# Optimization experiments

Hardware: AMD Instinct MI355X
Metric: run time of the kernel (lower is better)

## Reference

```python
import jax, jax.numpy as jnp
import numpy as np

HIDDEN = 2048
HEADS = 32
GROUPS = 8
HEAD_DIM = HIDDEN // HEADS  # 64
BSZ = 1
SEQ = 2048
KV_DIM = GROUPS * HEAD_DIM  # 512


def setup_inputs() -> dict:
    key = jax.random.key(0)
    ks = jax.random.split(key, 10)
    scale = 1.0 / np.sqrt(HIDDEN)
    x = jax.random.normal(ks[0], (BSZ, SEQ, HIDDEN), dtype=jnp.float32)
    # causal mask: 1 where attention is disallowed (strictly upper triangular)
    causal_mask = jnp.triu(jnp.ones((SEQ, SEQ), dtype=jnp.float32), k=1)
    Wq = jax.random.normal(ks[1], (HIDDEN, HIDDEN), dtype=jnp.float32) * scale
    bq = jnp.zeros((HIDDEN,), dtype=jnp.float32)
    Wk = jax.random.normal(ks[2], (HIDDEN, KV_DIM), dtype=jnp.float32) * scale
    bk = jnp.zeros((KV_DIM,), dtype=jnp.float32)
    Wv = jax.random.normal(ks[3], (HIDDEN, KV_DIM), dtype=jnp.float32) * scale
    bv = jnp.zeros((KV_DIM,), dtype=jnp.float32)
    Wo = jax.random.normal(ks[4], (HIDDEN, HIDDEN), dtype=jnp.float32) * scale
    bo = jnp.zeros((HIDDEN,), dtype=jnp.float32)
    return {"x": x, "causal_mask": causal_mask, "Wq": Wq, "bq": bq,
            "Wk": Wk, "bk": bk, "Wv": Wv, "bv": bv, "Wo": Wo, "bo": bo}


def reference(x, causal_mask, Wq, bq, Wk, bk, Wv, bv, Wo, bo):
    b, s, _ = x.shape
    r = HEADS // GROUPS  # queries per KV group
    # projections
    q = (x @ Wq + bq).reshape(b, s, HEADS, HEAD_DIM).transpose(0, 2, 1, 3)   # [b,H,s,d]
    k = (x @ Wk + bk).reshape(b, s, GROUPS, HEAD_DIM).transpose(0, 2, 1, 3)  # [b,G,s,d]
    v = (x @ Wv + bv).reshape(b, s, GROUPS, HEAD_DIM).transpose(0, 2, 1, 3)  # [b,G,s,d]
    # group query heads: head h belongs to group h // r (matches torch expand/reshape order)
    qg = q.reshape(b, GROUPS, r, s, HEAD_DIM)
    inv_sqrt_d = 1.0 / jnp.sqrt(jnp.float32(HEAD_DIM))
    # scores without physically expanding K/V across heads
    scores = jnp.einsum('bgrsd,bgtd->bgrst', qg, k) * inv_sqrt_d  # [b,G,r,s,t]
    scores = scores + causal_mask * (-1e9)
    attn = jax.nn.softmax(scores, axis=-1)
    out = jnp.einsum('bgrst,bgtd->bgrsd', attn, v)                 # [b,G,r,s,d]
    out = out.reshape(b, HEADS, s, HEAD_DIM).transpose(0, 2, 1, 3).reshape(b, s, HIDDEN)
    return out @ Wo + bo
```

## Files before the change

kernel.cpp:

```cpp
#include <hip/hip_runtime.h>

typedef __attribute__((ext_vector_type(8))) short short8;
typedef __attribute__((ext_vector_type(4))) float f32x4;
typedef unsigned short us4 __attribute__((ext_vector_type(4)));
typedef unsigned int u32x2 __attribute__((ext_vector_type(2)));

#define S_LEN 2048
#define HID   2048
#define KVD   512
#define NH    32
#define NG    8
#define HD    64

__device__ __forceinline__ float b2f(ushort u) {
  union { uint i; float f; } c; c.i = ((uint)u) << 16; return c.f;
}
__device__ __forceinline__ ushort f2b(float f) {
  union { float f; uint u; } c; c.f = f;
  uint u = c.u;
  uint r = (u + 0x7FFFu + ((u >> 16) & 1u)) >> 16;
  return (ushort)r;
}

__device__ __forceinline__ void gld_lds16(const ushort* g, short* l) {
  __builtin_amdgcn_global_load_lds(
      (const __attribute__((address_space(1))) void*)g,
      (__attribute__((address_space(3))) void*)l, 16, 0, 0);
}

__global__ __launch_bounds__(256) void detect_dtype(
    const uint* __restrict__ mask, int* __restrict__ flagp)
{
  __shared__ int s_f32;
  if (threadIdx.x == 0) s_f32 = 1;
  __syncthreads();
  int bad = 0;
  for (int i = threadIdx.x; i < 8192; i += 256) {
    const uint w = mask[i];
    if (w != 0u && w != 0x3F800000u) bad = 1;
  }
  if (bad) s_f32 = 0;
  __syncthreads();
  if (threadIdx.x == 0) *flagp = s_f32;
}

__global__ __launch_bounds__(256) void convert_x(
    const void* __restrict__ src, ushort* __restrict__ dst, int n,
    const int* __restrict__ flagp)
{
  const int i = (blockIdx.x * 256 + threadIdx.x) * 4;
  if (i >= n) return;
  if (*flagp) {
    const f32x4 v = *(const f32x4*)((const float*)src + i);
    us4 o;
    o.x = f2b(v.x); o.y = f2b(v.y); o.z = f2b(v.z); o.w = f2b(v.w);
    *(us4*)(dst + i) = o;
  } else {
    *(us4*)(dst + i) = *(const us4*)((const ushort*)src + i);
  }
}

__global__ __launch_bounds__(256) void transpose_any(
    const void* __restrict__ src, ushort* __restrict__ dst, int R, int C,
    const int* __restrict__ flagp)
{
  const int f32 = *flagp;
  __shared__ ushort tile[32][33];
  const int x  = blockIdx.x * 32 + threadIdx.x;
  const int y0 = blockIdx.y * 32;
  for (int i = threadIdx.y; i < 32; i += 8) {
    const size_t idx = (size_t)(y0 + i) * C + x;
    tile[i][threadIdx.x] = f32 ? f2b(((const float*)src)[idx])
                               : ((const ushort*)src)[idx];
  }
  __syncthreads();
  const int xo  = blockIdx.y * 32 + threadIdx.x;
  const int yo0 = blockIdx.x * 32;
  for (int i = threadIdx.y; i < 32; i += 8)
    dst[(size_t)(yo0 + i) * R + xo] = tile[threadIdx.x][i];
}

struct GemmRegions {
  const ushort* Bt[3];
  const void*   bias[3];
  void*         out[3];
  int   ldo[3];
  int   trans[3];
  int   outf32[3];
  float scale[3];
  int   colStart[3];
  int   colEnd[3];
};

__global__ __launch_bounds__(256) void gemm_bt_kernel(
    const ushort* __restrict__ A, int M, int K, GemmRegions rg,
    const int* __restrict__ flagp)
{
  __shared__ __align__(16) short As[2][128 * 32];
  __shared__ __align__(16) short Bs[2][128 * 32];

  const int tid  = threadIdx.x;
  const int wave = tid >> 6;
  const int lane = tid & 63;
  const int wm = wave & 1, wn = wave >> 1;
  const int quad = lane >> 4, l16 = lane & 15;

  const int rowBase = blockIdx.y * 128;
  const int colBase = blockIdx.x * 128;

  int ri = 0;
#pragma unroll
  for (int i = 0; i < 3; ++i)
    if (colBase >= rg.colStart[i] && colBase < rg.colEnd[i]) ri = i;

  const int colLocal0   = colBase - rg.colStart[ri];
  const ushort* BtBase  = rg.Bt[ri] + (size_t)colLocal0 * K;
  const void* bias      = rg.bias[ri];
  void* outp            = rg.out[ri];
  const int   ldo   = rg.ldo[ri];
  const int   trans = rg.trans[ri];
  const int   of32  = rg.outf32[ri];
  const float scale = rg.scale[ri];

  const int sRow = tid >> 2;
  const int sCol = (tid & 3) * 8;

  const ushort* a0 = A + (size_t)(rowBase + sRow) * K + sCol;
  const ushort* a1 = A + (size_t)(rowBase + sRow + 64) * K + sCol;
  const ushort* b0 = BtBase + (size_t)sRow * K + sCol;
  const ushort* b1 = BtBase + (size_t)(sRow + 64) * K + sCol;

  const int waveRow = wave * 16;

  f32x4 acc[4][4] = {};
  const int nt = K >> 5;

  gld_lds16(a0, &As[0][waveRow * 32]);
  gld_lds16(a1, &As[0][(waveRow + 64) * 32]);
  gld_lds16(b0, &Bs[0][waveRow * 32]);
  gld_lds16(b1, &Bs[0][(waveRow + 64) * 32]);
  __syncthreads();

  for (int t = 0; t < nt; ++t) {
    const int cur = t & 1;

    if (t + 1 < nt) {
      const int nb = cur ^ 1;
      const int k0 = (t + 1) * 32;
      gld_lds16(a0 + k0, &As[nb][waveRow * 32]);
      gld_lds16(a1 + k0, &As[nb][(waveRow + 64) * 32]);
      gld_lds16(b0 + k0, &Bs[nb][waveRow * 32]);
      gld_lds16(b1 + k0, &Bs[nb][(waveRow + 64) * 32]);
    }

    short8 af[4], bf[4];
#pragma unroll
    for (int mi = 0; mi < 4; ++mi)
      af[mi] = *(const short8*)&As[cur][(wm * 64 + mi * 16 + l16) * 32 + quad * 8];
#pragma unroll
    for (int ni = 0; ni < 4; ++ni)
      bf[ni] = *(const short8*)&Bs[cur][(wn * 64 + ni * 16 + l16) * 32 + quad * 8];

#pragma unroll
    for (int mi = 0; mi < 4; ++mi)
#pragma unroll
      for (int ni = 0; ni < 4; ++ni)
        acc[mi][ni] = __builtin_amdgcn_mfma_f32_16x16x32_bf16(
            af[mi], bf[ni], acc[mi][ni], 0, 0, 0);

    __syncthreads();
  }

  const int f32io = *flagp;

#pragma unroll
  for (int ni = 0; ni < 4; ++ni) {
    const int cl = wn * 64 + ni * 16 + l16;
    const float bv = f32io ? ((const float*)bias)[colLocal0 + cl]
                           : b2f(((const ushort*)bias)[colLocal0 + cl]);
#pragma unroll
    for (int mi = 0; mi < 4; ++mi) {
      const int row0 = rowBase + wm * 64 + mi * 16 + quad * 4;
#pragma unroll
      for (int r = 0; r < 4; ++r) {
        const float val = (acc[mi][ni][r] + bv) * scale;
        if (!trans) {
          const size_t off = (size_t)(row0 + r) * ldo + colLocal0 + cl;
          if (of32 && f32io) ((float*)outp)[off] = val;
          else               ((ushort*)outp)[off] = f2b(val);
        } else {
          ((ushort*)outp)[(size_t)(colLocal0 + cl) * M + row0 + r] = f2b(val);
        }
      }
    }
  }
}

#define PSTR 40

#define MFMA16(A, B, C) __builtin_amdgcn_mfma_f32_16x16x32_bf16(A, B, C, 0, 0, 0)

#define LOADKV(IT, K00, K01, K10, K11, V0, V1, V2, V3)                        \
  {                                                                           \
    int t0_ = (IT) * 32;                                                      \
    if (t0_ > S_LEN - 32) t0_ = S_LEN - 32;                                   \
    const ushort* kr0_ = Kb + (size_t)(t0_ + l16) * KVD + g * HD + quad * 8;  \
    const ushort* kr1_ = kr0_ + (size_t)16 * KVD;                             \
    K00 = *(const short8*)(kr0_);                                             \
    K01 = *(const short8*)(kr0_ + 32);                                        \
    K10 = *(const short8*)(kr1_);                                             \
    K11 = *(const short8*)(kr1_ + 32);                                        \
    const ushort* vr_ = Vt + (size_t)(g * 64 + l16) * S_LEN + t0_ + quad * 8; \
    V0 = *(const short8*)(vr_);                                               \
    V1 = *(const short8*)(vr_ + (size_t)16 * S_LEN);                          \
    V2 = *(const short8*)(vr_ + (size_t)32 * S_LEN);                          \
    V3 = *(const short8*)(vr_ + (size_t)48 * S_LEN);                          \
  }

#define COMPUTE(IT, K00, K01, K10, K11, V0, V1, V2, V3)                       \
  {                                                                           \
    const int t0_ = (IT) * 32;                                                \
    const bool edge_ = (IT) >= nfull;                                         \
    _Pragma("unroll")                                                         \
    for (int qf = 0; qf < 4; ++qf) {                                          \
      f32x4 z0 = {};                                                          \
      z0 = MFMA16(K00, qfB[qf][0], z0);                                       \
      z0 = MFMA16(K01, qfB[qf][1], z0);                                       \
      f32x4 z1 = {};                                                          \
      z1 = MFMA16(K10, qfB[qf][0], z1);                                       \
      z1 = MFMA16(K11, qfB[qf][1], z1);                                       \
      ushort p0[4], p1[4];                                                    \
      _Pragma("unroll")                                                       \
      for (int r = 0; r < 4; ++r) {                                           \
        float pv0 = __expf(z0[r]);                                            \
        float pv1 = __expf(z1[r]);                                            \
        if (edge_) {                                                          \
          const int qq_ = qbase + qf * 16 + l16;                              \
          if (t0_ + quad * 4 + r > qq_)      pv0 = 0.f;                       \
          if (t0_ + 16 + quad * 4 + r > qq_) pv1 = 0.f;                       \
        }                                                                     \
        p0[r] = f2b(pv0);                                                     \
        p1[r] = f2b(pv1);                                                     \
      }                                                                       \
      u32x2 w0, w1;                                                           \
      w0.x = (uint)p0[0] | ((uint)p0[1] << 16);                               \
      w0.y = (uint)p0[2] | ((uint)p0[3] << 16);                               \
      w1.x = (uint)p1[0] | ((uint)p1[1] << 16);                               \
      w1.y = (uint)p1[2] | ((uint)p1[3] << 16);                               \
      *(u32x2*)&pb[(qf * 16 + l16) * PSTR + quad * 4] = w0;                   \
      *(u32x2*)&pb[(qf * 16 + l16) * PSTR + 16 + quad * 4] = w1;              \
    }                                                                         \
    asm volatile("s_waitcnt lgkmcnt(0)" ::: "memory");                        \
    _Pragma("unroll")                                                         \
    for (int qf = 0; qf < 4; ++qf) {                                          \
      const short8 pa =                                                       \
          *(const short8*)&pb[(qf * 16 + l16) * PSTR + quad * 8];             \
      l_acc[qf] = MFMA16(pa, ones, l_acc[qf]);                                \
      o_acc[qf][0] = MFMA16(pa, V0, o_acc[qf][0]);                            \
      o_acc[qf][1] = MFMA16(pa, V1, o_acc[qf][1]);                            \
      o_acc[qf][2] = MFMA16(pa, V2, o_acc[qf][2]);                            \
      o_acc[qf][3] = MFMA16(pa, V3, o_acc[qf][3]);                            \
    }                                                                         \
  }

__global__ __launch_bounds__(256, 2) void attn_kernel(
    const ushort* __restrict__ Q, const ushort* __restrict__ Kb,
    const ushort* __restrict__ Vt, ushort* __restrict__ O)
{
  __shared__ __align__(16) short Pls[4][64 * PSTR];

  const int tid  = threadIdx.x;
  const int wave = tid >> 6;
  const int lane = tid & 63;
  const int quad = lane >> 4, l16 = lane & 15;

  const int h = blockIdx.y;
  const int g = h >> 2;
  const int qbase = blockIdx.x * 256 + wave * 64;

  short8 qfB[4][2];
#pragma unroll
  for (int qf = 0; qf < 4; ++qf) {
    const ushort* qr = Q + (size_t)(qbase + qf * 16 + l16) * HID + h * HD;
#pragma unroll
    for (int ks = 0; ks < 2; ++ks)
      qfB[qf][ks] = *(const short8*)(qr + ks * 32 + quad * 8);
  }

  short8 ones;
#pragma unroll
  for (int j = 0; j < 8; ++j) ones[j] = (short)0x3F80;

  f32x4 o_acc[4][4] = {};
  f32x4 l_acc[4] = {};

  short* pb = &Pls[wave][0];
  const int nfull = qbase >> 5;
  const int total = nfull + 2;

  short8 ka00, ka01, ka10, ka11, va0, va1, va2, va3;
  short8 kb00, kb01, kb10, kb11, vb0, vb1, vb2, vb3;

  LOADKV(0, ka00, ka01, ka10, ka11, va0, va1, va2, va3);
  for (int it = 0; it < total; it += 2) {
    LOADKV(it + 1, kb00, kb01, kb10, kb11, vb0, vb1, vb2, vb3);
    COMPUTE(it, ka00, ka01, ka10, ka11, va0, va1, va2, va3);
    LOADKV(it + 2, ka00, ka01, ka10, ka11, va0, va1, va2, va3);
    COMPUTE(it + 1, kb00, kb01, kb10, kb11, vb0, vb1, vb2, vb3);
  }

#pragma unroll
  for (int qf = 0; qf < 4; ++qf) {
    f32x4 linv;
#pragma unroll
    for (int r = 0; r < 4; ++r) linv[r] = 1.f / l_acc[qf][r];
#pragma unroll
    for (int df = 0; df < 4; ++df)
#pragma unroll
      for (int r = 0; r < 4; ++r)
        O[(size_t)(qbase + qf * 16 + quad * 4 + r) * HID + h * HD + df * 16 + l16]
            = f2b(o_acc[qf][df][r] * linv[r]);
  }
}

extern "C" void kernel_launch(void* const* d_in, const int* in_sizes, int n_in,
                              void* d_out, int out_size, void* d_ws, size_t ws_size,
                              hipStream_t stream) {
  (void)in_sizes; (void)n_in; (void)out_size; (void)ws_size;

  int* flagp = (int*)d_ws;
  ushort* base = (ushort*)d_ws + 16;
  const int M4 = 2048 * 2048;
  const int M1 = 512 * 2048;

  ushort* xb  = base;
  ushort* Wqt = xb  + M4;
  ushort* Wkt = Wqt + M4;
  ushort* Wvt = Wkt + M1;
  ushort* Qb  = Wvt + M1;
  ushort* Kb  = Qb  + M4;
  ushort* Vt  = Kb  + M1;
  ushort* Ob  = Wqt;
  ushort* Wot = Qb;

  detect_dtype<<<1, 256, 0, stream>>>((const uint*)d_in[1], flagp);
  convert_x<<<M4 / 1024, 256, 0, stream>>>(d_in[0], xb, M4, flagp);

  dim3 tb(32, 8);
  transpose_any<<<dim3(64, 64), tb, 0, stream>>>(d_in[2], Wqt, 2048, 2048, flagp);
  transpose_any<<<dim3(16, 64), tb, 0, stream>>>(d_in[4], Wkt, 2048, 512, flagp);
  transpose_any<<<dim3(16, 64), tb, 0, stream>>>(d_in[6], Wvt, 2048, 512, flagp);

  GemmRegions rq;
  rq.Bt[0] = Wqt; rq.bias[0] = d_in[3]; rq.out[0] = Qb; rq.ldo[0] = 2048;
  rq.trans[0] = 0; rq.outf32[0] = 0; rq.scale[0] = 0.125f;
  rq.colStart[0] = 0;    rq.colEnd[0] = 2048;
  rq.Bt[1] = Wkt; rq.bias[1] = d_in[5]; rq.out[1] = Kb; rq.ldo[1] = 512;
  rq.trans[1] = 0; rq.outf32[1] = 0; rq.scale[1] = 1.0f;
  rq.colStart[1] = 2048; rq.colEnd[1] = 2560;
  rq.Bt[2] = Wvt; rq.bias[2] = d_in[7]; rq.out[2] = Vt; rq.ldo[2] = 0;
  rq.trans[2] = 1; rq.outf32[2] = 0; rq.scale[2] = 1.0f;
  rq.colStart[2] = 2560; rq.colEnd[2] = 3072;
  gemm_bt_kernel<<<dim3(3072 / 128, 2048 / 128), 256, 0, stream>>>(
      xb, 2048, 2048, rq, flagp);

  attn_kernel<<<dim3(2048 / 256, NH), 256, 0, stream>>>(Qb, Kb, Vt, Ob);

  transpose_any<<<dim3(64, 64), tb, 0, stream>>>(d_in[8], Wot, 2048, 2048, flagp);

  GemmRegions ro;
  ro.Bt[0] = Wot; ro.bias[0] = d_in[9]; ro.out[0] = d_out; ro.ldo[0] = 2048;
  ro.trans[0] = 0; ro.outf32[0] = 1; ro.scale[0] = 1.0f;
  ro.colStart[0] = 0; ro.colEnd[0] = 2048;
  for (int i = 1; i < 3; ++i) {
    ro.Bt[i] = Wot; ro.bias[i] = d_in[9]; ro.out[i] = d_out; ro.ldo[i] = 2048;
    ro.trans[i] = 0; ro.outf32[i] = 1; ro.scale[i] = 1.0f;
    ro.colStart[i] = 0; ro.colEnd[i] = 0;
  }
  gemm_bt_kernel<<<dim3(2048 / 128, 2048 / 128), 256, 0, stream>>>(
      Ob, 2048, 2048, ro, flagp);
}
```

Measured before the change: 342.0 us.

## Batch two score phases before PV phases with double-buffered P in LDS

Splits the fused per-tile compute into a score/exp phase and a PV phase, and double-buffers the per-wave P tile in shared memory. Two QK tiles are processed back to back before a single LDS wait, then both PV accumulations run, so one lgkmcnt wait covers two tiles. K and V loads are issued separately to spread memory latency across the phases. This doubles the LDS footprint for P and changes register pressure, which could affect occupancy at two blocks per CU.

```diff
diff --git a/kernel.cpp b/kernel.cpp
--- a/kernel.cpp
+++ b/kernel.cpp
@@ -200,7 +200,7 @@
 
 #define MFMA16(A, B, C) __builtin_amdgcn_mfma_f32_16x16x32_bf16(A, B, C, 0, 0, 0)
 
-#define LOADKV(IT, K00, K01, K10, K11, V0, V1, V2, V3)                        \
+#define LOADK(IT, K00, K01, K10, K11)                                         \
   {                                                                           \
     int t0_ = (IT) * 32;                                                      \
     if (t0_ > S_LEN - 32) t0_ = S_LEN - 32;                                   \
@@ -210,6 +210,12 @@
     K01 = *(const short8*)(kr0_ + 32);                                        \
     K10 = *(const short8*)(kr1_);                                             \
     K11 = *(const short8*)(kr1_ + 32);                                        \
+  }
+
+#define LOADV(IT, V0, V1, V2, V3)                                             \
+  {                                                                           \
+    int t0_ = (IT) * 32;                                                      \
+    if (t0_ > S_LEN - 32) t0_ = S_LEN - 32;                                   \
     const ushort* vr_ = Vt + (size_t)(g * 64 + l16) * S_LEN + t0_ + quad * 8; \
     V0 = *(const short8*)(vr_);                                               \
     V1 = *(const short8*)(vr_ + (size_t)16 * S_LEN);                          \
@@ -217,7 +223,7 @@
     V3 = *(const short8*)(vr_ + (size_t)48 * S_LEN);                          \
   }
 
-#define COMPUTE(IT, K00, K01, K10, K11, V0, V1, V2, V3)                       \
+#define SPHASE(IT, K00, K01, K10, K11, PB)                                    \
   {                                                                           \
     const int t0_ = (IT) * 32;                                                \
     const bool edge_ = (IT) >= nfull;                                         \
@@ -247,14 +253,17 @@
       w0.y = (uint)p0[2] | ((uint)p0[3] << 16);                               \
       w1.x = (uint)p1[0] | ((uint)p1[1] << 16);                               \
       w1.y = (uint)p1[2] | ((uint)p1[3] << 16);                               \
-      *(u32x2*)&pb[(qf * 16 + l16) * PSTR + quad * 4] = w0;                   \
-      *(u32x2*)&pb[(qf * 16 + l16) * PSTR + 16 + quad * 4] = w1;              \
+      *(u32x2*)&PB[(qf * 16 + l16) * PSTR + quad * 4] = w0;                   \
+      *(u32x2*)&PB[(qf * 16 + l16) * PSTR + 16 + quad * 4] = w1;              \
     }                                                                         \
-    asm volatile("s_waitcnt lgkmcnt(0)" ::: "memory");                        \
+  }
+
+#define PVPHASE(V0, V1, V2, V3, PB)                                           \
+  {                                                                           \
     _Pragma("unroll")                                                         \
     for (int qf = 0; qf < 4; ++qf) {                                          \
       const short8 pa =                                                       \
-          *(const short8*)&pb[(qf * 16 + l16) * PSTR + quad * 8];             \
+          *(const short8*)&PB[(qf * 16 + l16) * PSTR + quad * 8];             \
       l_acc[qf] = MFMA16(pa, ones, l_acc[qf]);                                \
       o_acc[qf][0] = MFMA16(pa, V0, o_acc[qf][0]);                            \
       o_acc[qf][1] = MFMA16(pa, V1, o_acc[qf][1]);                            \
@@ -267,7 +276,7 @@
     const ushort* __restrict__ Q, const ushort* __restrict__ Kb,
     const ushort* __restrict__ Vt, ushort* __restrict__ O)
 {
-  __shared__ __align__(16) short Pls[4][64 * PSTR];
+  __shared__ __align__(16) short Pls[4][2][64 * PSTR];
 
   const int tid  = threadIdx.x;
   const int wave = tid >> 6;
@@ -294,19 +303,26 @@
   f32x4 o_acc[4][4] = {};
   f32x4 l_acc[4] = {};
 
-  short* pb = &Pls[wave][0];
+  short* pbA = &Pls[wave][0][0];
+  short* pbB = &Pls[wave][1][0];
   const int nfull = qbase >> 5;
   const int total = nfull + 2;
 
-  short8 ka00, ka01, ka10, ka11, va0, va1, va2, va3;
-  short8 kb00, kb01, kb10, kb11, vb0, vb1, vb2, vb3;
-
-  LOADKV(0, ka00, ka01, ka10, ka11, va0, va1, va2, va3);
+  short8 k000, k001, k010, k011, k100, k101, k110, k111;
+  short8 v00, v01, v02, v03, v10, v11, v12, v13;
+
+  LOADK(0, k000, k001, k010, k011);
+  LOADV(0, v00, v01, v02, v03);
   for (int it = 0; it < total; it += 2) {
-    LOADKV(it + 1, kb00, kb01, kb10, kb11, vb0, vb1, vb2, vb3);
-    COMPUTE(it, ka00, ka01, ka10, ka11, va0, va1, va2, va3);
-    LOADKV(it + 2, ka00, ka01, ka10, ka11, va0, va1, va2, va3);
-    COMPUTE(it + 1, kb00, kb01, kb10, kb11, vb0, vb1, vb2, vb3);
+    LOADK(it + 1, k100, k101, k110, k111);
+    SPHASE(it, k000, k001, k010, k011, pbA);
+    SPHASE(it + 1, k100, k101, k110, k111, pbB);
+    LOADK(it + 2, k000, k001, k010, k011);
+    LOADV(it + 1, v10, v11, v12, v13);
+    asm volatile("s_waitcnt lgkmcnt(0)" ::: "memory");
+    PVPHASE(v00, v01, v02, v03, pbA);
+    PVPHASE(v10, v11, v12, v13, pbB);
+    LOADV(it + 2, v00, v01, v02, v03);
   }
 
 #pragma unroll
```

After: 345.6 us. About the same (+1.1%).

## Merge prep kernels into one launch and fold Wo transpose into attention grid

Applied to the files above, without the earlier changes.

Replaces the dtype-detect, x-conversion and three weight-transpose launches with a single prep kernel that dispatches work by block index. The input dtype is now inferred inline from one mask element instead of scanning the mask and writing a flag. The Wo transpose is appended as extra blocks on the attention grid, so it runs beside attention instead of as its own launch. This cuts launch count and serial gaps, at the cost of a weaker dtype check and extra non-attention blocks competing for attention's occupancy.

```diff
diff --git a/kernel.cpp b/kernel.cpp
--- a/kernel.cpp
+++ b/kernel.cpp
@@ -22,62 +22,58 @@
   return (ushort)r;
 }
 
+__device__ __forceinline__ int is_f32(const uint* mask) {
+  return mask[1] == 0x3F800000u;
+}
+
 __device__ __forceinline__ void gld_lds16(const ushort* g, short* l) {
   __builtin_amdgcn_global_load_lds(
       (const __attribute__((address_space(1))) void*)g,
       (__attribute__((address_space(3))) void*)l, 16, 0, 0);
 }
 
-__global__ __launch_bounds__(256) void detect_dtype(
-    const uint* __restrict__ mask, int* __restrict__ flagp)
+__global__ __launch_bounds__(256) void prep_kernel(
+    const void* __restrict__ x,  const void* __restrict__ wq,
+    const void* __restrict__ wk, const void* __restrict__ wv,
+    const uint* __restrict__ mask,
+    ushort* __restrict__ xb,  ushort* __restrict__ Wqt,
+    ushort* __restrict__ Wkt, ushort* __restrict__ Wvt)
 {
-  __shared__ int s_f32;
-  if (threadIdx.x == 0) s_f32 = 1;
+  const int f32 = is_f32(mask);
+  const int b = blockIdx.x;
+
+  if (b < 4096) {
+    const int i = (b * 256 + threadIdx.x) * 4;
+    if (f32) {
+      const f32x4 v = *(const f32x4*)((const float*)x + i);
+      us4 o;
+      o.x = f2b(v.x); o.y = f2b(v.y); o.z = f2b(v.z); o.w = f2b(v.w);
+      *(us4*)(xb + i) = o;
+    } else {
+      *(us4*)(xb + i) = *(const us4*)((const ushort*)x + i);
+    }
+    return;
+  }
+
+  const void* src; ushort* dst; int C, bx, by;
+  if (b < 8192)      { const int t = b - 4096; src = wq; dst = Wqt; C = 2048; bx = t & 63; by = t >> 6; }
+  else if (b < 9216) { const int t = b - 8192; src = wk; dst = Wkt; C = 512;  bx = t & 15; by = t >> 4; }
+  else               { const int t = b - 9216; src = wv; dst = Wvt; C = 512;  bx = t & 15; by = t >> 4; }
+
+  __shared__ ushort tile[32][33];
+  const int tx = threadIdx.x & 31, ty = threadIdx.x >> 5;
+  const int xcol = bx * 32 + tx;
+  const int y0   = by * 32;
+  for (int i = ty; i < 32; i += 8) {
+    const size_t idx = (size_t)(y0 + i) * C + xcol;
+    tile[i][tx] = f32 ? f2b(((const float*)src)[idx])
+                      : ((const ushort*)src)[idx];
+  }
   __syncthreads();
-  int bad = 0;
-  for (int i = threadIdx.x; i < 8192; i += 256) {
-    const uint w = mask[i];
-    if (w != 0u && w != 0x3F800000u) bad = 1;
-  }
-  if (bad) s_f32 = 0;
-  __syncthreads();
-  if (threadIdx.x == 0) *flagp = s_f32;
-}
-
-__global__ __launch_bounds__(256) void convert_x(
-    const void* __restrict__ src, ushort* __restrict__ dst, int n,
-    const int* __restrict__ flagp)
-{
-  const int i = (blockIdx.x * 256 + threadIdx.x) * 4;
-  if (i >= n) return;
-  if (*flagp) {
-    const f32x4 v = *(const f32x4*)((const float*)src + i);
-    us4 o;
-    o.x = f2b(v.x); o.y = f2b(v.y); o.z = f2b(v.z); o.w = f2b(v.w);
-    *(us4*)(dst + i) = o;
-  } else {
-    *(us4*)(dst + i) = *(const us4*)((const ushort*)src + i);
-  }
-}
-
-__global__ __launch_bounds__(256) void transpose_any(
-    const void* __restrict__ src, ushort* __restrict__ dst, int R, int C,
-    const int* __restrict__ flagp)
-{
-  const int f32 = *flagp;
-  __shared__ ushort tile[32][33];
-  const int x  = blockIdx.x * 32 + threadIdx.x;
-  const int y0 = blockIdx.y * 32;
-  for (int i = threadIdx.y; i < 32; i += 8) {
-    const size_t idx = (size_t)(y0 + i) * C + x;
-    tile[i][threadIdx.x] = f32 ? f2b(((const float*)src)[idx])
-                               : ((const ushort*)src)[idx];
-  }
-  __syncthreads();
-  const int xo  = blockIdx.y * 32 + threadIdx.x;
-  const int yo0 = blockIdx.x * 32;
-  for (int i = threadIdx.y; i < 32; i += 8)
-    dst[(size_t)(yo0 + i) * R + xo] = tile[threadIdx.x][i];
+  const int xo  = by * 32 + tx;
+  const int yo0 = bx * 32;
+  for (int i = ty; i < 32; i += 8)
+    dst[(size_t)(yo0 + i) * 2048 + xo] = tile[tx][i];
 }
 
 struct GemmRegions {
@@ -94,7 +90,7 @@
 
 __global__ __launch_bounds__(256) void gemm_bt_kernel(
     const ushort* __restrict__ A, int M, int K, GemmRegions rg,
-    const int* __restrict__ flagp)
+    const uint* __restrict__ mask)
 {
   __shared__ __align__(16) short As[2][128 * 32];
   __shared__ __align__(16) short Bs[2][128 * 32];
@@ -171,7 +167,7 @@
     __syncthreads();
   }
 
-  const int f32io = *flagp;
+  const int f32io = is_f32(mask);
 
 #pragma unroll
   for (int ni = 0; ni < 4; ++ni) {
@@ -265,9 +261,32 @@
 
 __global__ __launch_bounds__(256, 2) void attn_kernel(
     const ushort* __restrict__ Q, const ushort* __restrict__ Kb,
-    const ushort* __restrict__ Vt, ushort* __restrict__ O)
+    const ushort* __restrict__ Vt, ushort* __restrict__ O,
+    const void* __restrict__ wo, const uint* __restrict__ mask,
+    ushort* __restrict__ Wot)
 {
   __shared__ __align__(16) short Pls[4][64 * PSTR];
+
+  if (blockIdx.y >= NH) {
+    const int f32 = is_f32(mask);
+    const int t = (blockIdx.y - NH) * 8 + blockIdx.x;
+    const int bx = t & 63, by = t >> 6;
+    __shared__ ushort tile[32][33];
+    const int tx = threadIdx.x & 31, ty = threadIdx.x >> 5;
+    const int xcol = bx * 32 + tx;
+    const int y0   = by * 32;
+    for (int i = ty; i < 32; i += 8) {
+      const size_t idx = (size_t)(y0 + i) * 2048 + xcol;
+      tile[i][tx] = f32 ? f2b(((const float*)wo)[idx])
+                        : ((const ushort*)wo)[idx];
+    }
+    __syncthreads();
+    const int xo  = by * 32 + tx;
+    const int yo0 = bx * 32;
+    for (int i = ty; i < 32; i += 8)
+      Wot[(size_t)(yo0 + i) * 2048 + xo] = tile[tx][i];
+    return;
+  }
 
   const int tid  = threadIdx.x;
   const int wave = tid >> 6;
@@ -328,7 +347,6 @@
                               hipStream_t stream) {
   (void)in_sizes; (void)n_in; (void)out_size; (void)ws_size;
 
-  int* flagp = (int*)d_ws;
   ushort* base = (ushort*)d_ws + 16;
   const int M4 = 2048 * 2048;
   const int M1 = 512 * 2048;
@@ -341,15 +359,12 @@
   ushort* Kb  = Qb  + M4;
   ushort* Vt  = Kb  + M1;
   ushort* Ob  = Wqt;
-  ushort* Wot = Qb;
-
-  detect_dtype<<<1, 256, 0, stream>>>((const uint*)d_in[1], flagp);
-  convert_x<<<M4 / 1024, 256, 0, stream>>>(d_in[0], xb, M4, flagp);
-
-  dim3 tb(32, 8);
-  transpose_any<<<dim3(64, 64), tb, 0, stream>>>(d_in[2], Wqt, 2048, 2048, flagp);
-  transpose_any<<<dim3(16, 64), tb, 0, stream>>>(d_in[4], Wkt, 2048, 512, flagp);
-  transpose_any<<<dim3(16, 64), tb, 0, stream>>>(d_in[6], Wvt, 2048, 512, flagp);
+  ushort* Wot = xb;
+
+  const uint* maskp = (const uint*)d_in[1];
+
+  prep_kernel<<<10240, 256, 0, stream>>>(
+      d_in[0], d_in[2], d_in[4], d_in[6], maskp, xb, Wqt, Wkt, Wvt);
 
   GemmRegions rq;
   rq.Bt[0] = Wqt; rq.bias[0] = d_in[3]; rq.out[0] = Qb; rq.ldo[0] = 2048;
@@ -362,11 +377,10 @@
   rq.trans[2] = 1; rq.outf32[2] = 0; rq.scale[2] = 1.0f;
   rq.colStart[2] = 2560; rq.colEnd[2] = 3072;
   gemm_bt_kernel<<<dim3(3072 / 128, 2048 / 128), 256, 0, stream>>>(
-      xb, 2048, 2048, rq, flagp);
-
-  attn_kernel<<<dim3(2048 / 256, NH), 256, 0, stream>>>(Qb, Kb, Vt, Ob);
-
-  transpose_any<<<dim3(64, 64), tb, 0, stream>>>(d_in[8], Wot, 2048, 2048, flagp);
+      xb, 2048, 2048, rq, maskp);
+
+  attn_kernel<<<dim3(2048 / 256, NH + 512), 256, 0, stream>>>(
+      Qb, Kb, Vt, Ob, d_in[8], maskp, Wot);
 
   GemmRegions ro;
   ro.Bt[0] = Wot; ro.bias[0] = d_in[9]; ro.out[0] = d_out; ro.ldo[0] = 2048;
@@ -378,5 +392,5 @@
     ro.colStart[i] = 0; ro.colEnd[i] = 0;
   }
   gemm_bt_kernel<<<dim3(2048 / 128, 2048 / 128), 256, 0, stream>>>(
-      Ob, 2048, 2048, ro, flagp);
-}
+      Ob, 2048, 2048, ro, maskp);
+}
```

Measured after the change: 313.5 us. 1.09x faster.
